# Kernel tuning notes

Measured on AMD Instinct MI355X. Metric: run time of the kernel, lower is better.

The kernel has to match this reference:

```python
import jax, jax.numpy as jnp
import numpy as np

HID = 256
B, H, W, Q = 4, 192, 192, 36864


def conv3x3(x, w, b):
    # x [B,C,H,W], w [O,C,3,3]
    y = jax.lax.conv_general_dilated(x, w, (1, 1), ((1, 1), (1, 1)),
                                     dimension_numbers=('NCHW', 'OIHW', 'NCHW'))
    return y + b[None, :, None, None]


def gather_nchw(x, iy, ix):
    # nearest-neighbor gather: x [B,C,H,W], iy/ix [B,Q] -> [B,Q,C]
    b, c, h, w = x.shape
    lin = iy * w + ix
    g = jnp.take_along_axis(x.reshape(b, c, h * w), lin[:, None, :], axis=2)
    return jnp.transpose(g, (0, 2, 1))


def bilinear_border(x, cy, cx):
    # grid_sample bilinear, padding_mode='border', align_corners=False
    b, c, h, w = x.shape
    fy = ((cy + 1.0) * h - 1.0) * 0.5
    fx = ((cx + 1.0) * w - 1.0) * 0.5
    y0 = jnp.floor(fy)
    x0 = jnp.floor(fx)
    wy = fy - y0
    wx = fx - x0
    y0i = jnp.clip(y0, 0, h - 1).astype(jnp.int32)
    y1i = jnp.clip(y0 + 1, 0, h - 1).astype(jnp.int32)
    x0i = jnp.clip(x0, 0, w - 1).astype(jnp.int32)
    x1i = jnp.clip(x0 + 1, 0, w - 1).astype(jnp.int32)
    v00 = gather_nchw(x, y0i, x0i)
    v01 = gather_nchw(x, y0i, x1i)
    v10 = gather_nchw(x, y1i, x0i)
    v11 = gather_nchw(x, y1i, x1i)
    wy = wy[..., None]
    wx = wx[..., None]
    return (v00 * (1 - wy) * (1 - wx) + v01 * (1 - wy) * wx
            + v10 * wy * (1 - wx) + v11 * wy * wx)


def setup_inputs():
    key = jax.random.key(0)
    ks = jax.random.split(key, 20)
    sc = 0.05
    d = {}
    d['inp'] = jax.random.normal(ks[0], (B, 3, H, W), jnp.float32)
    d['score'] = jax.random.normal(ks[1], (B, 3, H, W), jnp.float32)
    d['coord'] = jax.random.uniform(ks[2], (B, Q, 2), jnp.float32, -1.0, 1.0)
    d['cell'] = jnp.full((B, Q, 2), 2.0 / H, jnp.float32)
    d['coef_w'] = jax.random.normal(ks[3], (HID, 9, 3, 3), jnp.float32) * sc
    d['coef_b'] = jnp.zeros((HID,), jnp.float32)
    d['freq_w'] = jax.random.normal(ks[4], (HID, 9, 3, 3), jnp.float32) * sc
    d['freq_b'] = jnp.zeros((HID,), jnp.float32)
    d['phase_w'] = jax.random.normal(ks[5], (HID // 2, 2), jnp.float32) * sc  # Linear(2, HID//2, bias=False)
    d['a1_w'] = jax.random.normal(ks[6], (128, 3, 3, 3), jnp.float32) * sc
    d['a1_b'] = jnp.zeros((128,), jnp.float32)
    d['a2_w'] = jax.random.normal(ks[7], (3, 128, 3, 3), jnp.float32) * sc
    d['a2_b'] = jnp.zeros((3,), jnp.float32)
    dims = [HID, 256, 256, 256, 256, 3]
    for i in range(5):
        d[f'im_w{i}'] = jax.random.normal(ks[8 + i], (dims[i + 1], dims[i]), jnp.float32) * sc
        d[f'im_b{i}'] = jnp.zeros((dims[i + 1],), jnp.float32)
    return d


def lte_forward(inp, score, coord, cell,
                coef_w, coef_b, freq_w, freq_b, phase_w,
                a1_w, a1_b, a2_w, a2_b,
                im_w0, im_b0, im_w1, im_b1, im_w2, im_b2, im_w3, im_b3, im_w4, im_b4):
    # adapter: conv -> sin -> conv -> sin (Sine w0=1)
    weights = jnp.sin(conv3x3(jnp.sin(conv3x3(inp, a1_w, a1_b)), a2_w, a2_b))
    feat = jnp.concatenate([inp, score, weights], axis=1)  # [B,9,H,W]
    coef = conv3x3(feat, coef_w, coef_b)  # [B,HID,H,W]
    freq = conv3x3(feat, freq_w, freq_b)
    h, w = feat.shape[-2], feat.shape[-1]
    eps = 1e-6
    # single ensemble member (vx=vy=0): clamp coord and nearest-sample
    cy = jnp.clip(coord[..., 0], -1 + eps, 1 - eps)
    cx = jnp.clip(coord[..., 1], -1 + eps, 1 - eps)
    iy = jnp.clip(jnp.round(((cy + 1.0) * h - 1.0) * 0.5), 0, h - 1).astype(jnp.int32)
    ix = jnp.clip(jnp.round(((cx + 1.0) * w - 1.0) * 0.5), 0, w - 1).astype(jnp.int32)
    q_coef = gather_nchw(coef, iy, ix)  # [B,Q,HID]
    q_freq = gather_nchw(freq, iy, ix)  # [B,Q,HID]
    # nearest pixel-center coordinates (make_coord values)
    qy = -1.0 + (2.0 * iy.astype(jnp.float32) + 1.0) / h
    qx = -1.0 + (2.0 * ix.astype(jnp.float32) + 1.0) / w
    rel = jnp.stack([(coord[..., 0] - qy) * h, (coord[..., 1] - qx) * w], axis=-1)  # [B,Q,2]
    rel_cell = cell * jnp.asarray([h, w], jnp.float32)
    # split into (even,odd) frequency pairs: [B,Q,HID/2,2], contract with rel_coord
    qf = q_freq.reshape(q_freq.shape[0], q_freq.shape[1], HID // 2, 2)
    qf = jnp.einsum('bqjk,bqk->bqj', qf, rel)  # [B,Q,HID/2]
    qf = qf + jnp.einsum('bqk,jk->bqj', rel_cell, phase_w)  # phase linear, no bias
    qf = jnp.concatenate([jnp.cos(jnp.pi * qf), jnp.sin(jnp.pi * qf)], axis=-1)  # [B,Q,HID]
    x = q_coef * qf
    for lw, lb in ((im_w0, im_b0), (im_w1, im_b1), (im_w2, im_b2), (im_w3, im_b3)):
        x = jax.nn.relu(jnp.einsum('bqi,oi->bqo', x, lw) + lb)
    pred = jnp.einsum('bqi,oi->bqo', x, im_w4) + im_b4  # [B,Q,3]
    area = jnp.abs(rel[..., 0] * rel[..., 1]) + 1e-9
    ret = pred * (area / area)[..., None]  # single member -> weight 1 (kept for fidelity)
    ret = ret + bilinear_border(inp, coord[..., 0], coord[..., 1])
    return ret


def reference(inp, score, coord, cell,
              coef_w, coef_b, freq_w, freq_b, phase_w,
              a1_w, a1_b, a2_w, a2_b,
              im_w0, im_b0, im_w1, im_b1, im_w2, im_b2, im_w3, im_b3, im_w4, im_b4):
    return lte_forward(inp, score, coord, cell,
                       coef_w, coef_b, freq_w, freq_b, phase_w,
                       a1_w, a1_b, a2_w, a2_b,
                       im_w0, im_b0, im_w1, im_b1, im_w2, im_b2, im_w3, im_b3, im_w4, im_b4)
```

## Files before the change

### kernel.cpp

```cpp
#include <hip/hip_runtime.h>

typedef unsigned short u16;
typedef unsigned int   u32;
typedef unsigned long long u64;
typedef __attribute__((ext_vector_type(8))) short v8s;
typedef __attribute__((ext_vector_type(8))) unsigned short v8u;
typedef __attribute__((ext_vector_type(4))) float v4f;

#define PI_F 3.14159265358979323846f

__device__ __forceinline__ float bf2f(u16 v){ u32 u = ((u32)v) << 16; return __builtin_bit_cast(float, u); }
__device__ __forceinline__ u16 f2bf(float f){
    u32 u = __builtin_bit_cast(u32, f);
    u32 r = (u + 0x7fffu + ((u >> 16) & 1u)) >> 16;
    return (u16)r;
}
__device__ __forceinline__ bool is_f32(const void* cellp){
    u32 u = *(const u32*)cellp;
    return ((u >> 16) != (u & 0xffffu));
}
__device__ __forceinline__ float ldin(const void* p, int i, bool f32){
    return f32 ? ((const float*)p)[i] : bf2f(((const u16*)p)[i]);
}

#define FEAT16_OFF 0
#define W2P_OFF   4718592
#define A1W_OFF   4816896
#define A1B_OFF   4830720
#define A2W_OFF   4831232
#define A2B_OFF   4845056
#define PWF_OFF   4845312
#define IBF_OFF   4846336
#define IWC_OFF   4850688
#define CBP_OFF   5376512
#define W4P_OFF   5378560
#define W1SW_OFF  5386752
#define W2SW_OFF  5403136

__global__ __launch_bounds__(256) void k_pack(
    const void* cw, const void* fw, const void* a1w, const void* a1b,
    const void* a2w, const void* a2b, const void* cb, const void* fb, const void* pwp,
    const void* iw0, const void* ib0, const void* iw1, const void* ib1,
    const void* iw2, const void* ib2, const void* iw3, const void* ib3,
    const void* iw4, const void* ib4, const void* cellp, char* ws){
    bool f32 = is_f32(cellp);
    u16*   w2p  = (u16*)(ws + W2P_OFF);
    float* a1wf = (float*)(ws + A1W_OFF);
    float* a1bf = (float*)(ws + A1B_OFF);
    float* a2wf = (float*)(ws + A2W_OFF);
    float* a2bf = (float*)(ws + A2B_OFF);
    float* pwf  = (float*)(ws + PWF_OFF);
    float* ibf  = (float*)(ws + IBF_OFF);
    u16*   iwc  = (u16*)(ws + IWC_OFF);
    float* cbp  = (float*)(ws + CBP_OFF);
    u16*   w4p  = (u16*)(ws + W4P_OFF);
    u16*   w1sw = (u16*)(ws + W1SW_OFF);
    u16*   w2sw = (u16*)(ws + W2SW_OFF);

    int t = blockIdx.x*256 + threadIdx.x;
    if (t < 49152){
        int c = t >> 9, rem = t & 511;
        int tile = c/3, ks = c%3;
        int lm = rem >> 5, r2 = rem & 31, quad = r2 >> 3, jj = r2 & 7;
        int n = tile*16 + lm;
        int r = quad*8 + jj;
        u16 v = 0;
        if (r < 27){
            int pix = r/9, ch = r%9;
            int tap = ks*3 + pix;
            int src = ch*9 + tap;
            if (n < 256) v = f2bf(ldin(cw, n*81 + src, f32));
            else { int u_ = n - 256; int tt = u_ >> 4, nn = u_ & 15;
                   int f = 2*((tt>>1)*16 + nn) + (tt & 1);
                   v = f2bf(ldin(fw, f*81 + src, f32)); }
        }
        w2p[t] = v; return;
    }
    t -= 49152;
    if (t < 3456){ a1wf[t] = ldin(a1w, t, f32); return; }
    t -= 3456;
    if (t < 128){ a1bf[t] = ldin(a1b, t, f32); return; }
    t -= 128;
    if (t < 3456){
        int o = t/1152, r = t%1152, c = r/9, tap = r%9;
        a2wf[(o*9 + tap)*128 + c] = ldin(a2w, t, f32); return;
    }
    t -= 3456;
    if (t < 3){ a2bf[t] = ldin(a2b, t, f32); return; }
    t -= 3;
    if (t < 256){ pwf[t] = ldin(pwp, t, f32); return; }
    t -= 256;
    if (t < 1027){
        const void* src = (t < 256) ? ib0 : (t < 512) ? ib1 : (t < 768) ? ib2 : (t < 1024) ? ib3 : ib4;
        int idx = (t < 1024) ? (t & 255) : (t - 1024);
        ibf[t] = ldin(src, idx, f32); return;
    }
    t -= 1027;
    if (t < 262144){
        int c = t >> 9, rem = t & 511;
        int lm = rem >> 5, r2 = rem & 31, quad = r2 >> 3, jj = r2 & 7;
        int nt = c & 3, ks = (c >> 2) & 7, wv = (c >> 5) & 3, l = c >> 7;
        int col = wv*64 + nt*16 + lm;
        int k = ks*32 + quad*8 + jj;
        const void* src = (l==0) ? iw0 : (l==1) ? iw1 : (l==2) ? iw2 : iw3;
        iwc[t] = f2bf(ldin(src, col*256 + k, f32)); return;
    }
    t -= 262144;
    if (t < 768){ return; }
    t -= 768;
    if (t < 512){
        float v;
        if (t < 256) v = ldin(cb, t, f32);
        else { int u_ = t - 256; int tt = u_ >> 4, nn = u_ & 15;
               int f = 2*((tt>>1)*16 + nn) + (tt & 1); v = ldin(fb, f, f32); }
        cbp[t] = v; return;
    }
    t -= 512;
    if (t < 4096){
        int ks = t >> 9, rem = t & 511;
        int lm = rem >> 5, r2 = rem & 31, quad = r2 >> 3, jj = r2 & 7;
        int k = ks*32 + quad*8 + jj;
        w4p[t] = (lm < 3) ? f2bf(ldin(iw4, lm*256 + k, f32)) : (u16)0;
        return;
    }
    t -= 4096;
    if (t < 8192){
        int c = t >> 9, rem = t & 511;
        int lm = rem >> 5, r2 = rem & 31, quad = r2 >> 3, jj = r2 & 7;
        int h = c >> 3, nt = (c & 7) >> 1, ks = c & 1;
        int ch = h*64 + nt*16 + lm;
        int kk = quad*8 + jj;
        u16 v = 0;
        int jr = -1, r = 0;
        if (ks == 0){ jr = kk >> 4; r = kk & 15; }
        else if (kk < 16){ jr = 2; r = kk; }
        if (jr >= 0 && r < 12){
            int px = r >> 2, ci = r & 3;
            if (ci < 3) v = f2bf(ldin(a1w, ch*27 + ci*9 + jr*3 + px, f32));
        }
        w1sw[t] = v; return;
    }
    t -= 8192;
    if (t < 18432){
        int c = t >> 9, rem = t & 511;
        int lm = rem >> 5, r2 = rem & 31, quad = r2 >> 3, jj = r2 & 7;
        int h = c / 18, tap = (c % 18) >> 1, ks = c & 1;
        int k = ks*32 + quad*8 + jj;
        int ch = h*64 + k;
        u16 v = 0;
        if (lm < 3) v = f2bf(ldin(a2w, lm*1152 + ch*9 + tap, f32));
        w2sw[t] = v; return;
    }
}

__global__ __launch_bounds__(256, 3) void k_adapter(const void* __restrict__ inp, const void* __restrict__ score,
                                                    const void* __restrict__ cellp, char* __restrict__ ws){
    __shared__ __attribute__((aligned(16))) char smem[46480];
    bool f32 = is_f32(cellp);
    const float* a1bf = (const float*)(ws + A1B_OFF);
    const float* a2bf = (const float*)(ws + A2B_OFF);
    const u16*   w1sw = (const u16*)(ws + W1SW_OFF);
    const u16*   w2sw = (const u16*)(ws + W2SW_OFF);
    u16* feat16 = (u16*)(ws + FEAT16_OFF);

    int blk = blockIdx.x; int b = blk/288; int rem = blk%288;
    int ty0 = (rem/12)*8, tx0 = (rem%12)*16;
    int tid = threadIdx.x;
    u16* S   = (u16*)smem;
    u16* A   = (u16*)(smem + 1920);
    u16* hid = (u16*)(smem + 22000);

    if (tid < 240) ((u64*)smem)[tid] = 0ULL;
    __syncthreads();
    #pragma unroll 1
    for (int e = tid; e < 720; e += 256){
        int ci = e/240, r2 = e%240, hy = r2/20, hx = r2%20;
        int gy = ty0 - 2 + hy, gx = tx0 - 2 + hx;
        if (gy >= 0 && gy < 192 && gx >= 0 && gx < 192)
            S[(hy*20+hx)*4 + ci] = f2bf(ldin(inp, (b*3+ci)*36864 + gy*192 + gx, f32));
    }
    __syncthreads();
    #pragma unroll 1
    for (int p = tid; p < 193; p += 256){
        u64* drow = (u64*)(A + p*52);
        if (p < 180){
            int hy = p/18, hx = p%18;
            #pragma unroll
            for (int jr = 0; jr < 3; ++jr){
                const u64* srow = (const u64*)(S + ((hy+jr)*20 + hx)*4);
                u64 v0 = srow[0], v1 = srow[1], v2 = srow[2];
                drow[jr*4+0] = v0; drow[jr*4+1] = v1; drow[jr*4+2] = v2; drow[jr*4+3] = 0ULL;
            }
            drow[12] = 0ULL;
        } else {
            #pragma unroll
            for (int k = 0; k < 13; ++k) drow[k] = 0ULL;
        }
    }
    __syncthreads();

    const int wv = tid >> 6, ln = tid & 63;
    const int lm = ln & 15, quad = ln >> 4;
    const int laneoff = lm*32 + quad*8;

    float bias2 = (lm < 3) ? a2bf[lm] : 0.f;
    v4f acc2[2];
    acc2[0] = (v4f){bias2,bias2,bias2,bias2};
    acc2[1] = acc2[0];

    #pragma unroll 1
    for (int h = 0; h < 2; ++h){
        float bias1 = a1bf[h*64 + wv*16 + lm];
        v8s B0 = *(const v8s*)(w1sw + (h*8 + wv*2 + 0)*512 + laneoff);
        v8s B1 = *(const v8s*)(w1sw + (h*8 + wv*2 + 1)*512 + laneoff);
        #pragma unroll 4
        for (int mt = 0; mt < 12; ++mt){
            const u16* ar = A + (mt*16 + lm)*52 + quad*8;
            v8s a0 = *(const v8s*)(ar);
            v8s a1 = *(const v8s*)(ar + 32);
            v4f c = (v4f){bias1,bias1,bias1,bias1};
            c = __builtin_amdgcn_mfma_f32_16x16x32_bf16(a0, B0, c, 0,0,0);
            c = __builtin_amdgcn_mfma_f32_16x16x32_bf16(a1, B1, c, 0,0,0);
            #pragma unroll
            for (int r = 0; r < 4; ++r){
                int px = mt*16 + quad*4 + r;
                if (px < 180){
                    int hy = px/18, hx = px - hy*18;
                    int gy = ty0 - 1 + hy, gx = tx0 - 1 + hx;
                    bool ok = (gy >= 0) & (gy < 192) & (gx >= 0) & (gx < 192);
                    hid[px*68 + wv*16 + lm] = ok ? f2bf(__sinf(c[r])) : (u16)0;
                }
            }
        }
        __syncthreads();
        #pragma unroll 2
        for (int tap = 0; tap < 9; ++tap){
            int ty = tap/3, tx = tap%3;
            v8s Bt0 = *(const v8s*)(w2sw + ((h*9 + tap)*2 + 0)*512 + laneoff);
            v8s Bt1 = *(const v8s*)(w2sw + ((h*9 + tap)*2 + 1)*512 + laneoff);
            #pragma unroll
            for (int i = 0; i < 2; ++i){
                int py = wv*2 + i;
                const u16* hrow = hid + ((py+ty)*18 + lm + tx)*68;
                v8s a0 = *(const v8s*)(hrow + quad*8);
                v8s a1 = *(const v8s*)(hrow + 32 + quad*8);
                acc2[i] = __builtin_amdgcn_mfma_f32_16x16x32_bf16(a0, Bt0, acc2[i], 0,0,0);
                acc2[i] = __builtin_amdgcn_mfma_f32_16x16x32_bf16(a1, Bt1, acc2[i], 0,0,0);
            }
        }
        __syncthreads();
    }
    u16* out3 = S;
    if (lm < 3){
        #pragma unroll
        for (int i = 0; i < 2; ++i)
            #pragma unroll
            for (int r = 0; r < 4; ++r){
                int m = (wv*2 + i)*16 + quad*4 + r;
                out3[m*4 + lm] = f2bf(__sinf(acc2[i][r]));
            }
    }
    __syncthreads();
    if (tid < 128){
        int py = tid >> 4, px = tid & 15;
        int gy = ty0 + py, gx = tx0 + px;
        int pi = b*3*36864 + gy*192 + gx;
        v8u lo, hi;
        lo[0] = f2bf(ldin(inp, pi, f32));
        lo[1] = f2bf(ldin(inp, pi + 36864, f32));
        lo[2] = f2bf(ldin(inp, pi + 2*36864, f32));
        lo[3] = f2bf(ldin(score, pi, f32));
        lo[4] = f2bf(ldin(score, pi + 36864, f32));
        lo[5] = f2bf(ldin(score, pi + 2*36864, f32));
        lo[6] = out3[tid*4 + 0];
        lo[7] = out3[tid*4 + 1];
        hi[0] = out3[tid*4 + 2];
        hi[1]=hi[2]=hi[3]=hi[4]=hi[5]=hi[6]=hi[7]=0;
        u16* fp = feat16 + ((b*192 + gy)*192 + gx)*16;
        *(v8u*)fp = lo;
        *(v8u*)(fp + 8) = hi;
    }
}

__global__ __launch_bounds__(256, 4) void k_mega(const char* __restrict__ ws,
                                                 const void* __restrict__ inp,
                                                 const void* __restrict__ coord,
                                                 const void* __restrict__ cellp,
                                                 void* __restrict__ out){
    __shared__ __attribute__((aligned(16))) char smem[32768];
    bool f32 = is_f32(cellp);
    const u16*   feat16 = (const u16*)(ws + FEAT16_OFF);
    const u16*   w2p    = (const u16*)(ws + W2P_OFF);
    const float* pwf    = (const float*)(ws + PWF_OFF);
    const float* ibf    = (const float*)(ws + IBF_OFF);
    const u16*   iwc    = (const u16*)(ws + IWC_OFF);
    const float* cbp    = (const float*)(ws + CBP_OFF);
    const u16*   w4p    = (const u16*)(ws + W4P_OFF);

    const int tid = threadIdx.x;
    const int qg0 = blockIdx.x * 64;
    const int b = qg0 / 36864;

    {
        int q = tid >> 2, j = tid & 3;
        int qg = qg0 + q;
        u16* ap = (u16*)smem;
        float c0 = ldin(coord, qg*2, f32), c1 = ldin(coord, qg*2+1, f32);
        const float e = 1e-6f;
        float cy = fminf(fmaxf(c0, -1.f+e), 1.f-e);
        float cx = fminf(fmaxf(c1, -1.f+e), 1.f-e);
        int iy = (int)rintf(((cy+1.f)*192.f-1.f)*0.5f); iy = min(max(iy,0),191);
        int ix = (int)rintf(((cx+1.f)*192.f-1.f)*0.5f); ix = min(max(ix,0),191);
        if (j < 3){
            int yy = iy - 1 + j;
            bool yok = (yy >= 0) & (yy <= 191);
            union { u16 a[32]; v8u v[4]; } buf;
            #pragma unroll
            for (int c = 0; c < 32; ++c) buf.a[c] = 0;
            if (yok){
                const u16* base = feat16 + ((b*192 + yy)*192)*16;
                #pragma unroll
                for (int pix = 0; pix < 3; ++pix){
                    int xx = ix - 1 + pix;
                    if (xx >= 0 && xx <= 191){
                        const u16* s = base + xx*16;
                        v8u v = *(const v8u*)s;
                        u16 c8 = s[8];
                        #pragma unroll
                        for (int c = 0; c < 8; ++c) buf.a[pix*9+c] = v[c];
                        buf.a[pix*9+8] = c8;
                    }
                }
            }
            u16* dst = ap + q*96 + j*32;
            *(v8u*)(dst)      = buf.v[0];
            *(v8u*)(dst + 8)  = buf.v[1];
            *(v8u*)(dst + 16) = buf.v[2];
            *(v8u*)(dst + 24) = buf.v[3];
        }
    }
    __syncthreads();

    const int wv = tid >> 6, ln = tid & 63;
    const int lm = ln & 15, quad = ln >> 4;
    const int laneoff = lm*32 + quad*8;
    u16* X = (u16*)smem;

    float4 mm[4];
    #pragma unroll
    for (int r = 0; r < 4; ++r){
        int qg = qg0 + wv*16 + quad*4 + r;
        float c0 = ldin(coord, qg*2, f32), c1 = ldin(coord, qg*2+1, f32);
        const float e = 1e-6f;
        float cy = fminf(fmaxf(c0, -1.f+e), 1.f-e);
        float cx = fminf(fmaxf(c1, -1.f+e), 1.f-e);
        int iy = (int)rintf(((cy+1.f)*192.f-1.f)*0.5f); iy = min(max(iy,0),191);
        int ix = (int)rintf(((cx+1.f)*192.f-1.f)*0.5f); ix = min(max(ix,0),191);
        float qy = -1.f + (2.f*iy + 1.f)/192.f;
        float qx = -1.f + (2.f*ix + 1.f)/192.f;
        mm[r].x = (c0 - qy)*192.f; mm[r].y = (c1 - qx)*192.f;
        mm[r].z = ldin(cellp, qg*2, f32)*192.f; mm[r].w = ldin(cellp, qg*2+1, f32)*192.f;
    }

    {
        v8s afr[3];
        #pragma unroll
        for (int ks = 0; ks < 3; ++ks)
            afr[ks] = *(const v8s*)(smem + ((wv*16 + lm)*96 + ks*32 + quad*8)*2);
        float p0[8], p1[8];
        #pragma unroll
        for (int g = 0; g < 8; ++g){
            int j = g*16 + lm;
            p0[g] = pwf[2*j]; p1[g] = pwf[2*j+1];
        }
        v8s Bc0[3], Bc1[3], Bf0[3], Bf1[3];
        {
            const u16* p;
            p = w2p + 0*1536  + laneoff; Bc0[0]=*(const v8s*)p; Bc0[1]=*(const v8s*)(p+512); Bc0[2]=*(const v8s*)(p+1024);
            p = w2p + 8*1536  + laneoff; Bc1[0]=*(const v8s*)p; Bc1[1]=*(const v8s*)(p+512); Bc1[2]=*(const v8s*)(p+1024);
            p = w2p + 16*1536 + laneoff; Bf0[0]=*(const v8s*)p; Bf0[1]=*(const v8s*)(p+512); Bf0[2]=*(const v8s*)(p+1024);
            p = w2p + 17*1536 + laneoff; Bf1[0]=*(const v8s*)p; Bf1[1]=*(const v8s*)(p+512); Bf1[2]=*(const v8s*)(p+1024);
        }
        __syncthreads();
        #pragma unroll 1
        for (int g = 0; g < 8; ++g){
            float bb0 = cbp[g*16+lm], bb1 = cbp[(8+g)*16+lm];
            float bb2 = cbp[(16+2*g)*16+lm], bb3 = cbp[(17+2*g)*16+lm];
            v4f a0 = (v4f){bb0,bb0,bb0,bb0};
            v4f a1 = (v4f){bb1,bb1,bb1,bb1};
            v4f a2 = (v4f){bb2,bb2,bb2,bb2};
            v4f a3 = (v4f){bb3,bb3,bb3,bb3};
            #pragma unroll
            for (int ks = 0; ks < 3; ++ks){
                a0 = __builtin_amdgcn_mfma_f32_16x16x32_bf16(afr[ks], Bc0[ks], a0, 0,0,0);
                a1 = __builtin_amdgcn_mfma_f32_16x16x32_bf16(afr[ks], Bc1[ks], a1, 0,0,0);
                a2 = __builtin_amdgcn_mfma_f32_16x16x32_bf16(afr[ks], Bf0[ks], a2, 0,0,0);
                a3 = __builtin_amdgcn_mfma_f32_16x16x32_bf16(afr[ks], Bf1[ks], a3, 0,0,0);
            }
            if (g < 7){
                const u16* p;
                p = w2p + (g+1)*1536    + laneoff; Bc0[0]=*(const v8s*)p; Bc0[1]=*(const v8s*)(p+512); Bc0[2]=*(const v8s*)(p+1024);
                p = w2p + (9+g)*1536    + laneoff; Bc1[0]=*(const v8s*)p; Bc1[1]=*(const v8s*)(p+512); Bc1[2]=*(const v8s*)(p+1024);
                p = w2p + (18+2*g)*1536 + laneoff; Bf0[0]=*(const v8s*)p; Bf0[1]=*(const v8s*)(p+512); Bf0[2]=*(const v8s*)(p+1024);
                p = w2p + (19+2*g)*1536 + laneoff; Bf1[0]=*(const v8s*)p; Bf1[1]=*(const v8s*)(p+512); Bf1[2]=*(const v8s*)(p+1024);
            }
            int j = g*16 + lm;
            int koff_c = (j>>5)*2048 + (j&31);
            int koff_s = ((128+j)>>5)*2048 + (j&31);
            #pragma unroll
            for (int r = 0; r < 4; ++r){
                float qf = a2[r]*mm[r].x + a3[r]*mm[r].y + mm[r].z*p0[g] + mm[r].w*p1[g];
                float sn, cs;
                __sincosf(PI_F * qf, &sn, &cs);
                int q = wv*16 + quad*4 + r;
                X[koff_c + q*32] = f2bf(a0[r] * cs);
                X[koff_s + q*32] = f2bf(a1[r] * sn);
            }
        }
    }
    __syncthreads();

    #pragma unroll 1
    for (int l = 0; l < 4; ++l){
        const u16* Wb = iwc + (l*4 + wv)*16384 + laneoff;
        v4f acc[4][4];
        #pragma unroll
        for (int nt = 0; nt < 4; ++nt){
            float bv = ibf[l*256 + wv*64 + nt*16 + lm];
            #pragma unroll
            for (int mt = 0; mt < 4; ++mt) acc[nt][mt] = (v4f){bv,bv,bv,bv};
        }
        v8s bw[2][4];
        #pragma unroll
        for (int nt = 0; nt < 4; ++nt){
            bw[0][nt] = *(const v8s*)(Wb + (0*4 + nt)*512);
            bw[1][nt] = *(const v8s*)(Wb + (1*4 + nt)*512);
        }
        #pragma unroll
        for (int ks = 0; ks < 8; ++ks){
            v8s a[4];
            #pragma unroll
            for (int mt = 0; mt < 4; ++mt)
                a[mt] = *(const v8s*)(smem + (ks*2048 + (mt*16 + lm)*32 + quad*8)*2);
            v8s nb[4];
            if (ks < 6){
                #pragma unroll
                for (int nt = 0; nt < 4; ++nt)
                    nb[nt] = *(const v8s*)(Wb + ((ks+2)*4 + nt)*512);
            }
            #pragma unroll
            for (int nt = 0; nt < 4; ++nt)
                #pragma unroll
                for (int mt = 0; mt < 4; ++mt)
                    acc[nt][mt] = __builtin_amdgcn_mfma_f32_16x16x32_bf16(a[mt], bw[ks&1][nt], acc[nt][mt], 0,0,0);
            if (ks < 6){
                #pragma unroll
                for (int nt = 0; nt < 4; ++nt) bw[ks&1][nt] = nb[nt];
            }
        }
        __syncthreads();
        #pragma unroll
        for (int nt = 0; nt < 4; ++nt){
            int col = wv*64 + nt*16 + lm;
            u16* base = X + (col>>5)*2048 + (col&31);
            #pragma unroll
            for (int mt = 0; mt < 4; ++mt)
                #pragma unroll
                for (int r = 0; r < 4; ++r){
                    int q = mt*16 + quad*4 + r;
                    base[q*32] = f2bf(fmaxf(acc[nt][mt][r], 0.f));
                }
        }
        __syncthreads();
    }

    {
        float bv = (lm < 3) ? ibf[1024 + lm] : 0.f;
        v4f accf = (v4f){bv,bv,bv,bv};
        v8s bA = *(const v8s*)(w4p + laneoff);
        #pragma unroll
        for (int ks = 0; ks < 8; ++ks){
            v8s a = *(const v8s*)(smem + (ks*2048 + (wv*16 + lm)*32 + quad*8)*2);
            v8s bN;
            if (ks < 7) bN = *(const v8s*)(w4p + (ks+1)*512 + laneoff);
            accf = __builtin_amdgcn_mfma_f32_16x16x32_bf16(a, bA, accf, 0,0,0);
            bA = bN;
        }
        if (lm < 3){
            #pragma unroll
            for (int r = 0; r < 4; ++r){
                int q = wv*16 + quad*4 + r;
                int qg = qg0 + q;
                float c0 = ldin(coord, qg*2, f32), c1 = ldin(coord, qg*2+1, f32);
                float fy = ((c0 + 1.f)*192.f - 1.f)*0.5f;
                float fx = ((c1 + 1.f)*192.f - 1.f)*0.5f;
                float y0 = floorf(fy), x0 = floorf(fx);
                float wy = fy - y0, wx = fx - x0;
                int y0i = (int)fminf(fmaxf(y0, 0.f), 191.f);
                int y1i = (int)fminf(fmaxf(y0 + 1.f, 0.f), 191.f);
                int x0i = (int)fminf(fmaxf(x0, 0.f), 191.f);
                int x1i = (int)fminf(fmaxf(x0 + 1.f, 0.f), 191.f);
                int ibase = (b*3 + lm)*36864;
                float v00 = ldin(inp, ibase + y0i*192 + x0i, f32);
                float v01 = ldin(inp, ibase + y0i*192 + x1i, f32);
                float v10 = ldin(inp, ibase + y1i*192 + x0i, f32);
                float v11 = ldin(inp, ibase + y1i*192 + x1i, f32);
                float bil = v00*(1.f-wy)*(1.f-wx) + v01*(1.f-wy)*wx + v10*wy*(1.f-wx) + v11*wy*wx;
                float val = accf[r] + bil;
                if (f32) ((float*)out)[qg*3 + lm] = val;
                else     ((u16*)out)[qg*3 + lm] = f2bf(val);
            }
        }
    }
}

extern "C" void kernel_launch(void* const* d_in, const int* in_sizes, int n_in,
                              void* d_out, int out_size, void* d_ws, size_t ws_size,
                              hipStream_t stream){
    (void)in_sizes; (void)n_in; (void)out_size; (void)ws_size;
    const void* inp   = d_in[0];
    const void* score = d_in[1];
    const void* coord = d_in[2];
    const void* cellp = d_in[3];
    const void* cw    = d_in[4];
    const void* cb    = d_in[5];
    const void* fw    = d_in[6];
    const void* fb    = d_in[7];
    const void* pw    = d_in[8];
    const void* a1w   = d_in[9];
    const void* a1b   = d_in[10];
    const void* a2w   = d_in[11];
    const void* a2b   = d_in[12];
    const void* iw0   = d_in[13];
    const void* ib0   = d_in[14];
    const void* iw1   = d_in[15];
    const void* ib1   = d_in[16];
    const void* iw2   = d_in[17];
    const void* ib2   = d_in[18];
    const void* iw3   = d_in[19];
    const void* ib3   = d_in[20];
    const void* iw4   = d_in[21];
    const void* ib4   = d_in[22];
    char* ws = (char*)d_ws;

    hipLaunchKernelGGL(k_pack, dim3(1374), dim3(256), 0, stream,
                       cw, fw, a1w, a1b, a2w, a2b, cb, fb, pw,
                       iw0, ib0, iw1, ib1, iw2, ib2, iw3, ib3, iw4, ib4,
                       cellp, ws);
    hipLaunchKernelGGL(k_adapter, dim3(1152), dim3(256), 0, stream, inp, score, cellp, ws);
    hipLaunchKernelGGL(k_mega, dim3(2304), dim3(256), 0, stream, (const char*)ws, inp, coord, cellp, d_out);
}
```

Baseline: 350.3 us.

## Permute hidden-dim K order and XOR-swizzle LDS activations for packed 32-bit stores

```diff
diff --git a/kernel.cpp b/kernel.cpp
--- a/kernel.cpp
+++ b/kernel.cpp
@@ -21,6 +21,10 @@
 }
 __device__ __forceinline__ float ldin(const void* p, int i, bool f32){
     return f32 ? ((const float*)p)[i] : bf2f(((const u16*)p)[i]);
+}
+__device__ __forceinline__ int pminv(int kp){
+    int w2 = kp >> 6, p6 = kp & 63;
+    return w2*64 + ((((p6>>5)&1)*2 + (p6&1)))*16 + ((p6>>1)&15);
 }
 
 #define FEAT16_OFF 0
@@ -101,9 +105,12 @@
         int lm = rem >> 5, r2 = rem & 31, quad = r2 >> 3, jj = r2 & 7;
         int nt = c & 3, ks = (c >> 2) & 7, wv = (c >> 5) & 3, l = c >> 7;
         int col = wv*64 + nt*16 + lm;
-        int k = ks*32 + quad*8 + jj;
+        int kp = ks*32 + quad*8 + jj;
+        int kl;
+        if (l == 0) kl = (kp & 1) ? 128 + (kp >> 1) : (kp >> 1);
+        else        kl = pminv(kp);
         const void* src = (l==0) ? iw0 : (l==1) ? iw1 : (l==2) ? iw2 : iw3;
-        iwc[t] = f2bf(ldin(src, col*256 + k, f32)); return;
+        iwc[t] = f2bf(ldin(src, col*256 + kl, f32)); return;
     }
     t -= 262144;
     if (t < 768){ return; }
@@ -119,8 +126,9 @@
     if (t < 4096){
         int ks = t >> 9, rem = t & 511;
         int lm = rem >> 5, r2 = rem & 31, quad = r2 >> 3, jj = r2 & 7;
-        int k = ks*32 + quad*8 + jj;
-        w4p[t] = (lm < 3) ? f2bf(ldin(iw4, lm*256 + k, f32)) : (u16)0;
+        int kp = ks*32 + quad*8 + jj;
+        int kl = pminv(kp);
+        w4p[t] = (lm < 3) ? f2bf(ldin(iw4, lm*256 + kl, f32)) : (u16)0;
         return;
     }
     t -= 4096;
@@ -282,7 +290,7 @@
     }
 }
 
-__global__ __launch_bounds__(256, 4) void k_mega(const char* __restrict__ ws,
+__global__ __launch_bounds__(256, 3) void k_mega(const char* __restrict__ ws,
                                                  const void* __restrict__ inp,
                                                  const void* __restrict__ coord,
                                                  const void* __restrict__ cellp,
@@ -344,7 +352,7 @@
     const int wv = tid >> 6, ln = tid & 63;
     const int lm = ln & 15, quad = ln >> 4;
     const int laneoff = lm*32 + quad*8;
-    u16* X = (u16*)smem;
+    u32* X32 = (u32*)smem;
 
     float4 mm[4];
     #pragma unroll
@@ -404,17 +412,17 @@
                 p = w2p + (18+2*g)*1536 + laneoff; Bf0[0]=*(const v8s*)p; Bf0[1]=*(const v8s*)(p+512); Bf0[2]=*(const v8s*)(p+1024);
                 p = w2p + (19+2*g)*1536 + laneoff; Bf1[0]=*(const v8s*)p; Bf1[1]=*(const v8s*)(p+512); Bf1[2]=*(const v8s*)(p+1024);
             }
-            int j = g*16 + lm;
-            int koff_c = (j>>5)*2048 + (j&31);
-            int koff_s = ((128+j)>>5)*2048 + (j&31);
+            int c2 = g*16 + lm;
+            int C = c2 >> 2, sw = lm >> 2;
+            int abase = C*256 + (lm & 3);
             #pragma unroll
             for (int r = 0; r < 4; ++r){
                 float qf = a2[r]*mm[r].x + a3[r]*mm[r].y + mm[r].z*p0[g] + mm[r].w*p1[g];
                 float sn, cs;
                 __sincosf(PI_F * qf, &sn, &cs);
                 int q = wv*16 + quad*4 + r;
-                X[koff_c + q*32] = f2bf(a0[r] * cs);
-                X[koff_s + q*32] = f2bf(a1[r] * sn);
+                u32 val = (u32)f2bf(a0[r] * cs) | ((u32)f2bf(a1[r] * sn) << 16);
+                X32[abase + ((q ^ sw) << 2)] = val;
             }
         }
     }
@@ -441,7 +449,8 @@
             v8s a[4];
             #pragma unroll
             for (int mt = 0; mt < 4; ++mt)
-                a[mt] = *(const v8s*)(smem + (ks*2048 + (mt*16 + lm)*32 + quad*8)*2);
+                a[mt] = *(const v8s*)((const char*)smem +
+                        ((((ks*4 + quad)*64) + ((mt*16 + lm) ^ quad)) << 4));
             v8s nb[4];
             if (ks < 6){
                 #pragma unroll
@@ -460,15 +469,18 @@
         }
         __syncthreads();
         #pragma unroll
-        for (int nt = 0; nt < 4; ++nt){
-            int col = wv*64 + nt*16 + lm;
-            u16* base = X + (col>>5)*2048 + (col&31);
+        for (int h = 0; h < 2; ++h){
+            int c2 = wv*32 + h*16 + lm;
+            int C = c2 >> 2, sw = lm >> 2;
+            int abase = C*256 + (lm & 3);
             #pragma unroll
             for (int mt = 0; mt < 4; ++mt)
                 #pragma unroll
                 for (int r = 0; r < 4; ++r){
                     int q = mt*16 + quad*4 + r;
-                    base[q*32] = f2bf(fmaxf(acc[nt][mt][r], 0.f));
+                    u32 lo16 = f2bf(fmaxf(acc[2*h+0][mt][r], 0.f));
+                    u32 hi16 = f2bf(fmaxf(acc[2*h+1][mt][r], 0.f));
+                    X32[abase + ((q ^ sw) << 2)] = lo16 | (hi16 << 16);
                 }
         }
         __syncthreads();
@@ -480,7 +492,8 @@
         v8s bA = *(const v8s*)(w4p + laneoff);
         #pragma unroll
         for (int ks = 0; ks < 8; ++ks){
-            v8s a = *(const v8s*)(smem + (ks*2048 + (wv*16 + lm)*32 + quad*8)*2);
+            v8s a = *(const v8s*)((const char*)smem +
+                    ((((ks*4 + quad)*64) + ((wv*16 + lm) ^ quad)) << 4));
             v8s bN;
             if (ks < 7) bN = *(const v8s*)(w4p + (ks+1)*512 + laneoff);
             accf = __builtin_amdgcn_mfma_f32_16x16x32_bf16(a, bA, accf, 0,0,0);
```

Result: slower. 358.5 us (+2.3%).
